# Kernel optimization log

Measured on AMD Instinct MI355X. Metric: run time of the kernel, lower is better.

## Reference

```python
import jax, jax.numpy as jnp
import numpy as np

# ---- module hyperparameters (from init_kwargs) ----
DIM = 16        # Hilbert-space dimension (density matrix is DIM x DIM)
BATCH = 32      # number of initial states evolved in parallel
K_LIND = 4      # number of Lindblad collapse operators
N_TS = 512      # number of Euler integration steps
N_CTRLS = 4     # number of control channels
N_PARAMS = 16   # B-spline control points per channel
DEGREE = 3      # cubic B-splines
T_TOTAL = 1.0
DT = T_TOTAL / N_TS


def _bspline_basis_matrix(t, knots, degree):
    """Cox-de Boor recursion, vectorized over all basis functions.
    t: (n_ts,), knots: (n_knots,). Returns (n_ts, n_knots-1-degree)."""
    k = knots
    # degree-0: indicator of half-open knot spans -> (n_ts, n_knots-1)
    B = ((k[None, :-1] <= t[:, None]) & (t[:, None] < k[None, 1:])).astype(t.dtype)
    for d in range(1, degree + 1):
        left_den = k[d:-1] - k[:-(d + 1)]
        right_den = k[d + 1:] - k[1:-d]
        left = jnp.where(left_den > 0,
                         (t[:, None] - k[None, :-(d + 1)]) / jnp.where(left_den > 0, left_den, 1.0) * B[:, :-1],
                         0.0)
        right = jnp.where(right_den > 0,
                          (k[None, d + 1:] - t[:, None]) / jnp.where(right_den > 0, right_den, 1.0) * B[:, 1:],
                          0.0)
        B = left + right
    return B  # (n_ts, n_knots - 1 - degree) == (n_ts, N_PARAMS)


def setup_inputs() -> dict:
    key = jax.random.key(0)
    ks = jax.random.split(key, 10)
    f32 = jnp.float32
    params = 0.5 * jax.random.normal(ks[0], (N_PARAMS, N_CTRLS), f32)
    H0_re = jax.random.normal(ks[1], (DIM, DIM), f32)
    H0_im = jax.random.normal(ks[2], (DIM, DIM), f32)
    Hc_re = jax.random.normal(ks[3], (N_CTRLS, DIM, DIM), f32)
    Hc_im = jax.random.normal(ks[4], (N_CTRLS, DIM, DIM), f32)
    L_re = 0.3 * jax.random.normal(ks[5], (K_LIND, DIM, DIM), f32)
    L_im = 0.3 * jax.random.normal(ks[6], (K_LIND, DIM, DIM), f32)
    # valid density matrices: rho0 = A A^dag / tr(A A^dag)
    A = (jax.random.normal(ks[7], (BATCH, DIM, DIM), f32)
         + 1j * jax.random.normal(ks[8], (BATCH, DIM, DIM), f32)).astype(jnp.complex64)
    rho0 = jnp.einsum('bij,bkj->bik', A, A.conj())
    tr = jnp.trace(rho0, axis1=-2, axis2=-1).real[:, None, None]
    rho0 = rho0 / tr.astype(jnp.complex64)
    return {
        'params': params,
        'H0_re': H0_re, 'H0_im': H0_im,
        'Hc_re': Hc_re, 'Hc_im': Hc_im,
        'L_re': L_re, 'L_im': L_im,
        'rho0_re': jnp.real(rho0).astype(f32),
        'rho0_im': jnp.imag(rho0).astype(f32),
    }


def reference(params, H0_re, H0_im, Hc_re, Hc_im, L_re, L_im, rho0_re, rho0_im):
    c64 = jnp.complex64
    # Hermitize Hamiltonians
    H0 = (H0_re + 1j * H0_im).astype(c64)
    H0 = 0.5 * (H0 + H0.conj().T)
    Hc = (Hc_re + 1j * Hc_im).astype(c64)
    Hc = 0.5 * (Hc + jnp.conj(jnp.swapaxes(Hc, -1, -2)))
    L = (L_re + 1j * L_im).astype(c64)              # (K, d, d)
    LdL = jnp.einsum('kji,kjl->il', L.conj(), L)    # sum_k L^dag L  (d, d)
    rho0 = (rho0_re + 1j * rho0_im).astype(c64)     # (B, d, d)

    # B-spline control pulses (clamped knot vector, as in evaluate_bspline_batch)
    t = jnp.arange(N_TS, dtype=jnp.float32) * DT
    knots = jnp.concatenate([
        jnp.zeros(DEGREE, jnp.float32),
        jnp.linspace(0.0, T_TOTAL, N_PARAMS - DEGREE + 1).astype(jnp.float32),
        T_TOTAL * jnp.ones(DEGREE, jnp.float32),
    ])
    basis = _bspline_basis_matrix(t, knots, DEGREE)  # (n_ts, n_params)
    u = basis @ params                               # (n_ts, n_ctrls)

    def step(rho, u_t):
        H = H0 + jnp.einsum('c,cij->ij', u_t.astype(c64), Hc)
        jump = jnp.einsum('kij,bjl,kml->bim', L, rho, L.conj())
        drho = (-1j) * (H @ rho - rho @ H) + jump - 0.5 * (LdL @ rho + rho @ LdL)
        rho_new = rho + DT * drho
        pops = jnp.real(jnp.diagonal(rho_new, axis1=-2, axis2=-1)).astype(jnp.float32)
        return rho_new, pops

    _, pops = jax.lax.scan(step, rho0, u)
    return pops  # (n_ts, batch, dim) real populations
```

## Files before the change

### kernel.cpp

```cpp
#include <hip/hip_runtime.h>
#include <hip/hip_bf16.h>

#define DIM    16
#define BATCH  32
#define KL     4
#define NTS    512
#define NC     4
#define NPAR   16
#define DTF    (1.0f/512.0f)
#define BST    40
#define FST    20

using short8  = __attribute__((ext_vector_type(8))) short;
using short4v = __attribute__((ext_vector_type(4))) short;
using f32x4   = __attribute__((ext_vector_type(4))) float;

__device__ __forceinline__ float b2f(__hip_bfloat16 x) { return __bfloat162float(x); }

__device__ __forceinline__ float ldval(const void* p, int idx, bool isf32) {
  return isf32 ? ((const float*)p)[idx]
               : __bfloat162float(((const __hip_bfloat16*)p)[idx]);
}
__device__ __forceinline__ unsigned short f2bf(float x) {
  unsigned u = __float_as_uint(x);
  unsigned r = u + 0x7FFFu + ((u >> 16) & 1u);
  return (unsigned short)(r >> 16);
}
__device__ __forceinline__ float bf2f(unsigned short h) {
  return __uint_as_float(((unsigned)h) << 16);
}
__device__ __forceinline__ void split2(float v, unsigned short& h, unsigned short& l) {
  unsigned u = __float_as_uint(v);
  h = (unsigned short)(u >> 16);
  float r = v - __uint_as_float(u & 0xFFFF0000u);
  l = (unsigned short)(__float_as_uint(r) >> 16);
}
__device__ __forceinline__ short8 ldfrag(const unsigned short* p) {
  return *(const short8*)p;
}
__device__ __forceinline__ short8 negbf8(short8 a) {
  union { short8 s; unsigned u[4]; } v; v.s = a;
  #pragma unroll
  for (int q = 0; q < 4; ++q) v.u[q] ^= 0x80008000u;
  return v.s;
}
__device__ __forceinline__ f32x4 mm3(short8 Ah, short8 Al, short8 Bh, short8 Bl, f32x4 acc) {
  acc = __builtin_amdgcn_mfma_f32_16x16x32_bf16(Ah, Bh, acc, 0, 0, 0);
  acc = __builtin_amdgcn_mfma_f32_16x16x32_bf16(Al, Bh, acc, 0, 0, 0);
  acc = __builtin_amdgcn_mfma_f32_16x16x32_bf16(Ah, Bl, acc, 0, 0, 0);
  return acc;
}
__device__ __forceinline__ void packfrag(const float* v, short8& hi, short8& lo) {
  union { short8 s; unsigned short e[8]; } H, L;
  #pragma unroll
  for (int q = 0; q < 8; ++q) split2(v[q], H.e[q], L.e[q]);
  hi = H.s; lo = L.s;
}

__global__ __launch_bounds__(512, 1)
void lindblad_evolve(const void* __restrict__ g_params,
                     const void* __restrict__ g_H0re, const void* __restrict__ g_H0im,
                     const void* __restrict__ g_Hcre, const void* __restrict__ g_Hcim,
                     const void* __restrict__ g_Lre,  const void* __restrict__ g_Lim,
                     const void* __restrict__ g_r0re, const void* __restrict__ g_r0im,
                     float* __restrict__ g_out)
{
  __shared__ __align__(16) unsigned short sPh[16*BST], sPl[16*BST];
  __shared__ __align__(16) unsigned short sTh[KL][16*BST], sTl[KL][16*BST];
  __shared__ __align__(16) unsigned short sLh[KL][16*BST], sLl[KL][16*BST];
  __shared__ __align__(16) float sMr[16*FST],  sMi[16*FST];
  __shared__ __align__(16) float sMrT[16*FST], sMiT[16*FST];
  __shared__ __align__(16) float sU[NTS][NC];
  __shared__ __align__(16) float sPops[NTS*DIM];
  __shared__ int sFlag;

  const int tid = threadIdx.x;
  const int b   = blockIdx.x;
  const int wv  = tid >> 6;
  const int ln  = tid & 63;
  const int fm  = ln & 15;
  const int fq  = ln >> 4;
  const int row0 = fq * 4;
  const int fOff  = fm*BST + fq*8;
  const int fOffS = fm*BST + ((fq*8 + 16) & 31);

  if (tid == 0) sFlag = 0;
  __syncthreads();
  if (tid < 256) {
    float v = b2f(((const __hip_bfloat16*)g_H0re)[tid]);
    if (!(fabsf(v) <= 1e10f)) atomicOr(&sFlag, 1);
  }
  __syncthreads();
  const bool isf32 = (sFlag != 0);

  {
    float kn[20];
    kn[0] = 0.f; kn[1] = 0.f; kn[2] = 0.f;
    #pragma unroll
    for (int q = 0; q < 14; ++q) kn[3 + q] = (float)q / 13.0f;
    kn[17] = 1.f; kn[18] = 1.f; kn[19] = 1.f;
    const float t = (float)tid * DTF;
    float B[19];
    #pragma unroll
    for (int q = 0; q < 19; ++q) B[q] = (kn[q] <= t && t < kn[q+1]) ? 1.f : 0.f;
    #pragma unroll
    for (int d = 1; d <= 3; ++d) {
      #pragma unroll
      for (int q = 0; q + d < 19; ++q) {
        float ld = kn[q+d]   - kn[q];
        float rd = kn[q+d+1] - kn[q+1];
        float lv = (ld > 0.f) ? (t - kn[q])     / ld * B[q]   : 0.f;
        float rv = (rd > 0.f) ? (kn[q+d+1] - t) / rd * B[q+1] : 0.f;
        B[q] = lv + rv;
      }
    }
    #pragma unroll
    for (int c = 0; c < NC; ++c) {
      float s = 0.f;
      #pragma unroll
      for (int q = 0; q < NPAR; ++q) s += B[q] * ldval(g_params, q*NC + c, isf32);
      sU[tid][c] = s;
    }
  }

  if (tid < 256) {
    float* scr = sPops;
    const int i = tid >> 4, j = tid & 15;
    const int ij = i*16 + j, ji = j*16 + i;
    float h0r = 0.5f * (ldval(g_H0re, ij, isf32) + ldval(g_H0re, ji, isf32));
    float h0i = 0.5f * (ldval(g_H0im, ij, isf32) - ldval(g_H0im, ji, isf32));
    float ldr = 0.f, ldi = 0.f;
    for (int k = 0; k < KL; ++k) {
      #pragma unroll
      for (int m = 0; m < DIM; ++m) {
        float ar = ldval(g_Lre, k*256 + m*16 + i, isf32), ai = ldval(g_Lim, k*256 + m*16 + i, isf32);
        float br = ldval(g_Lre, k*256 + m*16 + j, isf32), bi = ldval(g_Lim, k*256 + m*16 + j, isf32);
        ldr += ar*br + ai*bi;
        ldi += ar*bi - ai*br;
      }
    }
    scr[0*256 + ij] =  h0i - 0.5f*ldr;
    scr[1*256 + ij] = -h0r - 0.5f*ldi;
    #pragma unroll
    for (int c = 0; c < NC; ++c) {
      float hr = 0.5f * (ldval(g_Hcre, c*256 + ij, isf32) + ldval(g_Hcre, c*256 + ji, isf32));
      float hi = 0.5f * (ldval(g_Hcim, c*256 + ij, isf32) - ldval(g_Hcim, c*256 + ji, isf32));
      scr[(2 + 2*c)*256 + ij] =  hi;
      scr[(3 + 2*c)*256 + ij] = -hr;
    }
    #pragma unroll
    for (int k = 0; k < KL; ++k) {
      float lr = ldval(g_Lre, k*256 + ij, isf32);
      float li = ldval(g_Lim, k*256 + ij, isf32);
      unsigned short h;
      h = f2bf(lr); sLh[k][i*BST + j]      = h; sLl[k][i*BST + j]      = f2bf(lr - bf2f(h));
      h = f2bf(li); sLh[k][i*BST + 16 + j] = h; sLl[k][i*BST + 16 + j] = f2bf(li - bf2f(h));
    }
    float r0 = ldval(g_r0re, b*256 + ij, isf32);
    float m0 = ldval(g_r0im, b*256 + ij, isf32);
    unsigned short h, l;
    split2(r0, h, l); sPh[j*BST + i]      = h; sPl[j*BST + i]      = l;
    split2(m0, h, l); sPh[j*BST + 16 + i] = h; sPl[j*BST + 16 + i] = l;
  }

  __syncthreads();

  short8 Ah, Al;
  short8 TrBh, TrBl, TiBh, TiBl;
  short8 JBh[KL], JBl[KL];
  float  G0v[8], Gcv[NC][8];
  float  rm[4] = {0.f,0.f,0.f,0.f};

  if (wv < 2) {
    const int comp = (fq < 2) ? 0 : 1;
    const int base = (fq & 1) * 8;
    const float* scr = sPops;
    {
      const float* s0 = &scr[comp*256 + fm*16 + base];
      f32x4 va = *(const f32x4*)s0, vb = *(const f32x4*)(s0 + 4);
      #pragma unroll
      for (int q = 0; q < 4; ++q) { G0v[q] = va[q]; G0v[4+q] = vb[q]; }
    }
    #pragma unroll
    for (int c = 0; c < NC; ++c) {
      const float* s0 = &scr[(2 + 2*c + comp)*256 + fm*16 + base];
      f32x4 va = *(const f32x4*)s0, vb = *(const f32x4*)(s0 + 4);
      #pragma unroll
      for (int q = 0; q < 4; ++q) { Gcv[c][q] = va[q]; Gcv[c][4+q] = vb[q]; }
    }
    f32x4 uv = *(const f32x4*)&sU[0][0];
    float gv[8];
    #pragma unroll
    for (int q = 0; q < 8; ++q)
      gv[q] = G0v[q] + uv[0]*Gcv[0][q] + uv[1]*Gcv[1][q] + uv[2]*Gcv[2][q] + uv[3]*Gcv[3][q];
    packfrag(gv, Ah, Al);
  } else if (wv < 6) {
    const int k = wv - 2;
    TiBh = ldfrag(&sLh[k][fOff]);
    TiBl = ldfrag(&sLl[k][fOff]);
    TrBh = (fq >= 2) ? negbf8(TiBh) : TiBh;
    TrBl = (fq >= 2) ? negbf8(TiBl) : TiBl;
  } else if (wv == 6) {
    #pragma unroll
    for (int k = 0; k < KL; ++k) { JBh[k] = ldfrag(&sLh[k][fOff]); JBl[k] = ldfrag(&sLl[k][fOff]); }
    #pragma unroll
    for (int q = 0; q < 4; ++q) rm[q] = ldval(g_r0re, b*256 + (row0+q)*16 + fm, isf32);
  } else {
    #pragma unroll
    for (int k = 0; k < KL; ++k) {
      short8 h = ldfrag(&sLh[k][fOffS]);
      short8 l = ldfrag(&sLl[k][fOffS]);
      if (fq < 2) { h = negbf8(h); l = negbf8(l); }
      JBh[k] = h; JBl[k] = l;
    }
    #pragma unroll
    for (int q = 0; q < 4; ++q) rm[q] = ldval(g_r0im, b*256 + (row0+q)*16 + fm, isf32);
  }

  #pragma unroll 1
  for (int t = 0; t < NTS; ++t) {
    __syncthreads();

    if (wv < 2) {
      short8 Bh, Bl;
      if (wv == 0) {
        Bh = ldfrag(&sPh[fOff]);  Bl = ldfrag(&sPl[fOff]);
        if (fq >= 2) { Bh = negbf8(Bh); Bl = negbf8(Bl); }
      } else {
        Bh = ldfrag(&sPh[fOffS]); Bl = ldfrag(&sPl[fOffS]);
      }
      f32x4 a = {0.f,0.f,0.f,0.f};
      a = mm3(Ah, Al, Bh, Bl, a);
      float* Mn = (wv == 0) ? sMr  : sMi;
      float* Mt = (wv == 0) ? sMrT : sMiT;
      #pragma unroll
      for (int r = 0; r < 4; ++r) Mn[(row0 + r)*FST + fm] = a[r];
      *(f32x4*)&Mt[fm*FST + row0] = a;
    } else if (wv < 6) {
      const int k = wv - 2;
      short8 Arh = ldfrag(&sPh[fOff]),  Arl = ldfrag(&sPl[fOff]);
      short8 Aih = ldfrag(&sPh[fOffS]), Ail = ldfrag(&sPl[fOffS]);
      f32x4 tr = {0.f,0.f,0.f,0.f}, ti = {0.f,0.f,0.f,0.f};
      tr = mm3(Arh, Arl, TrBh, TrBl, tr);
      ti = mm3(Aih, Ail, TiBh, TiBl, ti);
      union { short4v s; unsigned short e[4]; } HR, LR, HI, LI;
      #pragma unroll
      for (int r = 0; r < 4; ++r) {
        split2(tr[r], HR.e[r], LR.e[r]);
        split2(ti[r], HI.e[r], LI.e[r]);
      }
      *(short4v*)&sTh[k][fm*BST + row0]      = HR.s;
      *(short4v*)&sTl[k][fm*BST + row0]      = LR.s;
      *(short4v*)&sTh[k][fm*BST + 16 + row0] = HI.s;
      *(short4v*)&sTl[k][fm*BST + 16 + row0] = LI.s;
    }

    __syncthreads();

    if (wv >= 6) {
      short8 T0h = ldfrag(&sTh[0][fOff]), T0l = ldfrag(&sTl[0][fOff]);
      short8 T1h = ldfrag(&sTh[1][fOff]), T1l = ldfrag(&sTl[1][fOff]);
      short8 T2h = ldfrag(&sTh[2][fOff]), T2l = ldfrag(&sTl[2][fOff]);
      short8 T3h = ldfrag(&sTh[3][fOff]), T3l = ldfrag(&sTl[3][fOff]);
      f32x4 a0 = {0.f,0.f,0.f,0.f}, a1 = {0.f,0.f,0.f,0.f},
            a2 = {0.f,0.f,0.f,0.f}, a3 = {0.f,0.f,0.f,0.f};
      a0 = mm3(JBh[0], JBl[0], T0h, T0l, a0);
      a1 = mm3(JBh[1], JBl[1], T1h, T1l, a1);
      a2 = mm3(JBh[2], JBl[2], T2h, T2l, a2);
      a3 = mm3(JBh[3], JBl[3], T3h, T3l, a3);
      const float* Mt = (wv == 6) ? sMrT : sMiT;
      const float* Mn = (wv == 6) ? sMr  : sMi;
      f32x4 d1 = *(const f32x4*)&Mt[fm*FST + row0];
      f32x4 d2 = *(const f32x4*)&Mn[fm*FST + row0];
      union { short4v s; unsigned short e[4]; } HH, LL;
      if (wv == 6) {
        #pragma unroll
        for (int q = 0; q < 4; ++q) {
          rm[q] += DTF * (d1[q] + d2[q] + ((a0[q] + a1[q]) + (a2[q] + a3[q])));
          split2(rm[q], HH.e[q], LL.e[q]);
        }
        *(short4v*)&sPh[fm*BST + row0] = HH.s;
        *(short4v*)&sPl[fm*BST + row0] = LL.s;
        if ((unsigned)(fm - row0) < 4u) sPops[t*DIM + fm] = rm[fm - row0];
      } else {
        #pragma unroll
        for (int q = 0; q < 4; ++q) {
          rm[q] += DTF * (d1[q] - d2[q] - ((a0[q] + a1[q]) + (a2[q] + a3[q])));
          split2(rm[q], HH.e[q], LL.e[q]);
        }
        *(short4v*)&sPh[fm*BST + 16 + row0] = HH.s;
        *(short4v*)&sPl[fm*BST + 16 + row0] = LL.s;
      }
    } else if (wv < 2) {
      const int tn = (t + 1 < NTS) ? (t + 1) : t;
      f32x4 uv = *(const f32x4*)&sU[tn][0];
      float gv[8];
      #pragma unroll
      for (int q = 0; q < 8; ++q)
        gv[q] = G0v[q] + uv[0]*Gcv[0][q] + uv[1]*Gcv[1][q] + uv[2]*Gcv[2][q] + uv[3]*Gcv[3][q];
      packfrag(gv, Ah, Al);
    }
  }

  __syncthreads();
  #pragma unroll
  for (int s = 0; s < NTS*DIM/(512*4); ++s) {
    int idx = (s*512 + tid) * 4;
    int tt = idx >> 4, dd = idx & 15;
    *(float4*)&g_out[tt*(BATCH*DIM) + b*DIM + dd] = *(const float4*)&sPops[idx];
  }
}

extern "C" void kernel_launch(void* const* d_in, const int* in_sizes, int n_in,
                              void* d_out, int out_size, void* d_ws, size_t ws_size,
                              hipStream_t stream) {
  (void)out_size; (void)d_ws; (void)ws_size;
  const void *P, *H0r, *H0i, *Hcr, *Hci, *Lr, *Li, *R0r, *R0i;
  int idx64 = -1;
  for (int q = 0; q < n_in; ++q) if (in_sizes[q] == 64) idx64 = q;
  if (idx64 == 6) {
    H0i = d_in[0]; H0r = d_in[1];
    Hci = d_in[2]; Hcr = d_in[3];
    Li  = d_in[4]; Lr  = d_in[5];
    P   = d_in[6];
    R0i = d_in[7]; R0r = d_in[8];
  } else {
    P   = d_in[0];
    H0r = d_in[1]; H0i = d_in[2];
    Hcr = d_in[3]; Hci = d_in[4];
    Lr  = d_in[5]; Li  = d_in[6];
    R0r = d_in[7]; R0i = d_in[8];
  }
  lindblad_evolve<<<dim3(BATCH), dim3(512), 0, stream>>>(
      P, H0r, H0i, Hcr, Hci, Lr, Li, R0r, R0i, (float*)d_out);
}
```

Baseline: 416.4 us.

## Collapse eight specialised waves into two waves each doing all step stages

Reduces the block from 512 to 128 threads so that two waves each handle a real or imaginary component through the commutator, jump-operator transposes and accumulation, instead of eight role-specialised waves. This lowers the cost of each per-step __syncthreads and lets the commutator result stay in registers, removing the transposed staging buffer. It also replaces the scalar bf16 hi/lo split with byte-permute packing. In exchange, each wave does more serial MFMA work per step, so the dependency chain inside a step gets longer.

```diff
diff --git a/kernel.cpp b/kernel.cpp
--- a/kernel.cpp
+++ b/kernel.cpp
@@ -50,14 +50,34 @@
   acc = __builtin_amdgcn_mfma_f32_16x16x32_bf16(Ah, Bl, acc, 0, 0, 0);
   return acc;
 }
-__device__ __forceinline__ void packfrag(const float* v, short8& hi, short8& lo) {
-  union { short8 s; unsigned short e[8]; } H, L;
+__device__ __forceinline__ void pack4(f32x4 v, short4v& hi, short4v& lo) {
+  union { short4v s; unsigned d[2]; } H, L;
+  unsigned u0 = __float_as_uint(v[0]), u1 = __float_as_uint(v[1]);
+  unsigned u2 = __float_as_uint(v[2]), u3 = __float_as_uint(v[3]);
+  H.d[0] = __builtin_amdgcn_perm(u1, u0, 0x07060302u);
+  H.d[1] = __builtin_amdgcn_perm(u3, u2, 0x07060302u);
+  float r0 = v[0] - __uint_as_float(u0 & 0xFFFF0000u);
+  float r1 = v[1] - __uint_as_float(u1 & 0xFFFF0000u);
+  float r2 = v[2] - __uint_as_float(u2 & 0xFFFF0000u);
+  float r3 = v[3] - __uint_as_float(u3 & 0xFFFF0000u);
+  L.d[0] = __builtin_amdgcn_perm(__float_as_uint(r1), __float_as_uint(r0), 0x07060302u);
+  L.d[1] = __builtin_amdgcn_perm(__float_as_uint(r3), __float_as_uint(r2), 0x07060302u);
+  hi = H.s; lo = L.s;
+}
+__device__ __forceinline__ void pack8(const float* v, short8& hi, short8& lo) {
+  union { short8 s; unsigned d[4]; } H, L;
   #pragma unroll
-  for (int q = 0; q < 8; ++q) split2(v[q], H.e[q], L.e[q]);
+  for (int j = 0; j < 4; ++j) {
+    unsigned ua = __float_as_uint(v[2*j]), ub = __float_as_uint(v[2*j+1]);
+    H.d[j] = __builtin_amdgcn_perm(ub, ua, 0x07060302u);
+    float ra = v[2*j]   - __uint_as_float(ua & 0xFFFF0000u);
+    float rb = v[2*j+1] - __uint_as_float(ub & 0xFFFF0000u);
+    L.d[j] = __builtin_amdgcn_perm(__float_as_uint(rb), __float_as_uint(ra), 0x07060302u);
+  }
   hi = H.s; lo = L.s;
 }
 
-__global__ __launch_bounds__(512, 1)
+__global__ __launch_bounds__(128, 1)
 void lindblad_evolve(const void* __restrict__ g_params,
                      const void* __restrict__ g_H0re, const void* __restrict__ g_H0im,
                      const void* __restrict__ g_Hcre, const void* __restrict__ g_Hcim,
@@ -68,8 +88,7 @@
   __shared__ __align__(16) unsigned short sPh[16*BST], sPl[16*BST];
   __shared__ __align__(16) unsigned short sTh[KL][16*BST], sTl[KL][16*BST];
   __shared__ __align__(16) unsigned short sLh[KL][16*BST], sLl[KL][16*BST];
-  __shared__ __align__(16) float sMr[16*FST],  sMi[16*FST];
-  __shared__ __align__(16) float sMrT[16*FST], sMiT[16*FST];
+  __shared__ __align__(16) float sMr[16*FST], sMi[16*FST];
   __shared__ __align__(16) float sU[NTS][NC];
   __shared__ __align__(16) float sPops[NTS*DIM];
   __shared__ int sFlag;
@@ -86,20 +105,20 @@
 
   if (tid == 0) sFlag = 0;
   __syncthreads();
-  if (tid < 256) {
-    float v = b2f(((const __hip_bfloat16*)g_H0re)[tid]);
+  for (int e = tid; e < 256; e += 128) {
+    float v = b2f(((const __hip_bfloat16*)g_H0re)[e]);
     if (!(fabsf(v) <= 1e10f)) atomicOr(&sFlag, 1);
   }
   __syncthreads();
   const bool isf32 = (sFlag != 0);
 
-  {
+  for (int t0 = tid; t0 < NTS; t0 += 128) {
     float kn[20];
     kn[0] = 0.f; kn[1] = 0.f; kn[2] = 0.f;
     #pragma unroll
     for (int q = 0; q < 14; ++q) kn[3 + q] = (float)q / 13.0f;
     kn[17] = 1.f; kn[18] = 1.f; kn[19] = 1.f;
-    const float t = (float)tid * DTF;
+    const float t = (float)t0 * DTF;
     float B[19];
     #pragma unroll
     for (int q = 0; q < 19; ++q) B[q] = (kn[q] <= t && t < kn[q+1]) ? 1.f : 0.f;
@@ -119,13 +138,13 @@
       float s = 0.f;
       #pragma unroll
       for (int q = 0; q < NPAR; ++q) s += B[q] * ldval(g_params, q*NC + c, isf32);
-      sU[tid][c] = s;
-    }
-  }
-
-  if (tid < 256) {
+      sU[t0][c] = s;
+    }
+  }
+
+  for (int e = tid; e < 256; e += 128) {
     float* scr = sPops;
-    const int i = tid >> 4, j = tid & 15;
+    const int i = e >> 4, j = e & 15;
     const int ij = i*16 + j, ji = j*16 + i;
     float h0r = 0.5f * (ldval(g_H0re, ij, isf32) + ldval(g_H0re, ji, isf32));
     float h0i = 0.5f * (ldval(g_H0im, ij, isf32) - ldval(g_H0im, ji, isf32));
@@ -166,12 +185,8 @@
   __syncthreads();
 
   short8 Ah, Al;
-  short8 TrBh, TrBl, TiBh, TiBl;
-  short8 JBh[KL], JBl[KL];
   float  G0v[8], Gcv[NC][8];
-  float  rm[4] = {0.f,0.f,0.f,0.f};
-
-  if (wv < 2) {
+  {
     const int comp = (fq < 2) ? 0 : 1;
     const int base = (fq & 1) * 8;
     const float* scr = sPops;
@@ -193,14 +208,22 @@
     #pragma unroll
     for (int q = 0; q < 8; ++q)
       gv[q] = G0v[q] + uv[0]*Gcv[0][q] + uv[1]*Gcv[1][q] + uv[2]*Gcv[2][q] + uv[3]*Gcv[3][q];
-    packfrag(gv, Ah, Al);
-  } else if (wv < 6) {
-    const int k = wv - 2;
-    TiBh = ldfrag(&sLh[k][fOff]);
-    TiBl = ldfrag(&sLl[k][fOff]);
-    TrBh = (fq >= 2) ? negbf8(TiBh) : TiBh;
-    TrBl = (fq >= 2) ? negbf8(TiBl) : TiBl;
-  } else if (wv == 6) {
+    pack8(gv, Ah, Al);
+  }
+
+  short8 TiBh[2], TiBl[2], TrBh[2], TrBl[2];
+  #pragma unroll
+  for (int j = 0; j < 2; ++j) {
+    const int k = 2*wv + j;
+    TiBh[j] = ldfrag(&sLh[k][fOff]);
+    TiBl[j] = ldfrag(&sLl[k][fOff]);
+    TrBh[j] = (fq >= 2) ? negbf8(TiBh[j]) : TiBh[j];
+    TrBl[j] = (fq >= 2) ? negbf8(TiBl[j]) : TiBl[j];
+  }
+
+  short8 JBh[KL], JBl[KL];
+  float  rm[4];
+  if (wv == 0) {
     #pragma unroll
     for (int k = 0; k < KL; ++k) { JBh[k] = ldfrag(&sLh[k][fOff]); JBl[k] = ldfrag(&sLl[k][fOff]); }
     #pragma unroll
@@ -217,95 +240,96 @@
     for (int q = 0; q < 4; ++q) rm[q] = ldval(g_r0im, b*256 + (row0+q)*16 + fm, isf32);
   }
 
+  float* const Mn = (wv == 0) ? sMr : sMi;
+
   #pragma unroll 1
   for (int t = 0; t < NTS; ++t) {
     __syncthreads();
 
-    if (wv < 2) {
-      short8 Bh, Bl;
-      if (wv == 0) {
-        Bh = ldfrag(&sPh[fOff]);  Bl = ldfrag(&sPl[fOff]);
-        if (fq >= 2) { Bh = negbf8(Bh); Bl = negbf8(Bl); }
-      } else {
-        Bh = ldfrag(&sPh[fOffS]); Bl = ldfrag(&sPl[fOffS]);
+    short8 Pfh = ldfrag(&sPh[fOff]),  Pfl = ldfrag(&sPl[fOff]);
+    short8 Psh = ldfrag(&sPh[fOffS]), Psl = ldfrag(&sPl[fOffS]);
+
+    short8 MBh, MBl;
+    if (wv == 0) {
+      MBh = Pfh; MBl = Pfl;
+      if (fq >= 2) { MBh = negbf8(MBh); MBl = negbf8(MBl); }
+    } else {
+      MBh = Psh; MBl = Psl;
+    }
+    f32x4 mAcc = {0.f,0.f,0.f,0.f};
+    mAcc = mm3(Ah, Al, MBh, MBl, mAcc);
+
+    #pragma unroll
+    for (int j = 0; j < 2; ++j) {
+      const int k = 2*wv + j;
+      f32x4 tr = {0.f,0.f,0.f,0.f}, ti = {0.f,0.f,0.f,0.f};
+      tr = mm3(Pfh, Pfl, TrBh[j], TrBl[j], tr);
+      ti = mm3(Psh, Psl, TiBh[j], TiBl[j], ti);
+      short4v HR, LR, HI2, LI2;
+      pack4(tr, HR, LR);
+      pack4(ti, HI2, LI2);
+      *(short4v*)&sTh[k][fm*BST + row0]      = HR;
+      *(short4v*)&sTl[k][fm*BST + row0]      = LR;
+      *(short4v*)&sTh[k][fm*BST + 16 + row0] = HI2;
+      *(short4v*)&sTl[k][fm*BST + 16 + row0] = LI2;
+    }
+
+    #pragma unroll
+    for (int r = 0; r < 4; ++r) Mn[(row0 + r)*FST + fm] = mAcc[r];
+
+    __syncthreads();
+
+    short8 T0h = ldfrag(&sTh[0][fOff]), T0l = ldfrag(&sTl[0][fOff]);
+    short8 T1h = ldfrag(&sTh[1][fOff]), T1l = ldfrag(&sTl[1][fOff]);
+    short8 T2h = ldfrag(&sTh[2][fOff]), T2l = ldfrag(&sTl[2][fOff]);
+    short8 T3h = ldfrag(&sTh[3][fOff]), T3l = ldfrag(&sTl[3][fOff]);
+    f32x4 d2 = *(const f32x4*)&Mn[fm*FST + row0];
+    f32x4 a0 = {0.f,0.f,0.f,0.f}, a1 = {0.f,0.f,0.f,0.f},
+          a2 = {0.f,0.f,0.f,0.f}, a3 = {0.f,0.f,0.f,0.f};
+    a0 = mm3(JBh[0], JBl[0], T0h, T0l, a0);
+    a1 = mm3(JBh[1], JBl[1], T1h, T1l, a1);
+    a2 = mm3(JBh[2], JBl[2], T2h, T2l, a2);
+    a3 = mm3(JBh[3], JBl[3], T3h, T3l, a3);
+
+    short4v HH, LL;
+    if (wv == 0) {
+      f32x4 rv;
+      #pragma unroll
+      for (int q = 0; q < 4; ++q) {
+        rm[q] += DTF * (mAcc[q] + d2[q] + ((a0[q] + a1[q]) + (a2[q] + a3[q])));
+        rv[q] = rm[q];
       }
-      f32x4 a = {0.f,0.f,0.f,0.f};
-      a = mm3(Ah, Al, Bh, Bl, a);
-      float* Mn = (wv == 0) ? sMr  : sMi;
-      float* Mt = (wv == 0) ? sMrT : sMiT;
-      #pragma unroll
-      for (int r = 0; r < 4; ++r) Mn[(row0 + r)*FST + fm] = a[r];
-      *(f32x4*)&Mt[fm*FST + row0] = a;
-    } else if (wv < 6) {
-      const int k = wv - 2;
-      short8 Arh = ldfrag(&sPh[fOff]),  Arl = ldfrag(&sPl[fOff]);
-      short8 Aih = ldfrag(&sPh[fOffS]), Ail = ldfrag(&sPl[fOffS]);
-      f32x4 tr = {0.f,0.f,0.f,0.f}, ti = {0.f,0.f,0.f,0.f};
-      tr = mm3(Arh, Arl, TrBh, TrBl, tr);
-      ti = mm3(Aih, Ail, TiBh, TiBl, ti);
-      union { short4v s; unsigned short e[4]; } HR, LR, HI, LI;
-      #pragma unroll
-      for (int r = 0; r < 4; ++r) {
-        split2(tr[r], HR.e[r], LR.e[r]);
-        split2(ti[r], HI.e[r], LI.e[r]);
+      pack4(rv, HH, LL);
+      *(short4v*)&sPh[fm*BST + row0] = HH;
+      *(short4v*)&sPl[fm*BST + row0] = LL;
+      if ((unsigned)(fm - row0) < 4u) sPops[t*DIM + fm] = rm[fm - row0];
+    } else {
+      f32x4 rv;
+      #pragma unroll
+      for (int q = 0; q < 4; ++q) {
+        rm[q] += DTF * (mAcc[q] - d2[q] - ((a0[q] + a1[q]) + (a2[q] + a3[q])));
+        rv[q] = rm[q];
       }
-      *(short4v*)&sTh[k][fm*BST + row0]      = HR.s;
-      *(short4v*)&sTl[k][fm*BST + row0]      = LR.s;
-      *(short4v*)&sTh[k][fm*BST + 16 + row0] = HI.s;
-      *(short4v*)&sTl[k][fm*BST + 16 + row0] = LI.s;
-    }
-
-    __syncthreads();
-
-    if (wv >= 6) {
-      short8 T0h = ldfrag(&sTh[0][fOff]), T0l = ldfrag(&sTl[0][fOff]);
-      short8 T1h = ldfrag(&sTh[1][fOff]), T1l = ldfrag(&sTl[1][fOff]);
-      short8 T2h = ldfrag(&sTh[2][fOff]), T2l = ldfrag(&sTl[2][fOff]);
-      short8 T3h = ldfrag(&sTh[3][fOff]), T3l = ldfrag(&sTl[3][fOff]);
-      f32x4 a0 = {0.f,0.f,0.f,0.f}, a1 = {0.f,0.f,0.f,0.f},
-            a2 = {0.f,0.f,0.f,0.f}, a3 = {0.f,0.f,0.f,0.f};
-      a0 = mm3(JBh[0], JBl[0], T0h, T0l, a0);
-      a1 = mm3(JBh[1], JBl[1], T1h, T1l, a1);
-      a2 = mm3(JBh[2], JBl[2], T2h, T2l, a2);
-      a3 = mm3(JBh[3], JBl[3], T3h, T3l, a3);
-      const float* Mt = (wv == 6) ? sMrT : sMiT;
-      const float* Mn = (wv == 6) ? sMr  : sMi;
-      f32x4 d1 = *(const f32x4*)&Mt[fm*FST + row0];
-      f32x4 d2 = *(const f32x4*)&Mn[fm*FST + row0];
-      union { short4v s; unsigned short e[4]; } HH, LL;
-      if (wv == 6) {
-        #pragma unroll
-        for (int q = 0; q < 4; ++q) {
-          rm[q] += DTF * (d1[q] + d2[q] + ((a0[q] + a1[q]) + (a2[q] + a3[q])));
-          split2(rm[q], HH.e[q], LL.e[q]);
-        }
-        *(short4v*)&sPh[fm*BST + row0] = HH.s;
-        *(short4v*)&sPl[fm*BST + row0] = LL.s;
-        if ((unsigned)(fm - row0) < 4u) sPops[t*DIM + fm] = rm[fm - row0];
-      } else {
-        #pragma unroll
-        for (int q = 0; q < 4; ++q) {
-          rm[q] += DTF * (d1[q] - d2[q] - ((a0[q] + a1[q]) + (a2[q] + a3[q])));
-          split2(rm[q], HH.e[q], LL.e[q]);
-        }
-        *(short4v*)&sPh[fm*BST + 16 + row0] = HH.s;
-        *(short4v*)&sPl[fm*BST + 16 + row0] = LL.s;
-      }
-    } else if (wv < 2) {
+      pack4(rv, HH, LL);
+      *(short4v*)&sPh[fm*BST + 16 + row0] = HH;
+      *(short4v*)&sPl[fm*BST + 16 + row0] = LL;
+    }
+
+    {
       const int tn = (t + 1 < NTS) ? (t + 1) : t;
       f32x4 uv = *(const f32x4*)&sU[tn][0];
       float gv[8];
       #pragma unroll
       for (int q = 0; q < 8; ++q)
         gv[q] = G0v[q] + uv[0]*Gcv[0][q] + uv[1]*Gcv[1][q] + uv[2]*Gcv[2][q] + uv[3]*Gcv[3][q];
-      packfrag(gv, Ah, Al);
+      pack8(gv, Ah, Al);
     }
   }
 
   __syncthreads();
   #pragma unroll
-  for (int s = 0; s < NTS*DIM/(512*4); ++s) {
-    int idx = (s*512 + tid) * 4;
+  for (int s = 0; s < NTS*DIM/(128*4); ++s) {
+    int idx = (s*128 + tid) * 4;
     int tt = idx >> 4, dd = idx & 15;
     *(float4*)&g_out[tt*(BATCH*DIM) + b*DIM + dd] = *(const float4*)&sPops[idx];
   }
@@ -331,6 +355,6 @@
     Lr  = d_in[5]; Li  = d_in[6];
     R0r = d_in[7]; R0i = d_in[8];
   }
-  lindblad_evolve<<<dim3(BATCH), dim3(512), 0, stream>>>(
+  lindblad_evolve<<<dim3(BATCH), dim3(128), 0, stream>>>(
       P, H0r, H0i, Hcr, Hci, Lr, Li, R0r, R0i, (float*)d_out);
 }
```

Result: slower. 564.2 us (+35.5%).

## Interleave two batch states per block to overlap dependent phases

Applied to the files above, without the earlier changes.

Each block now evolves two density matrices. Phase 1 of one state runs between the same barriers as phase 2 of the other, so waves that sat idle during a serial dependency now have work. The grid is halved to 16 blocks, and the scalar bf16 split routines are replaced with byte-permute packing helpers. The cost is doubled shared memory for the buffers and populations, plus a longer serial chain per block.

```diff
diff --git a/kernel.cpp b/kernel.cpp
--- a/kernel.cpp
+++ b/kernel.cpp
@@ -50,10 +50,30 @@
   acc = __builtin_amdgcn_mfma_f32_16x16x32_bf16(Ah, Bl, acc, 0, 0, 0);
   return acc;
 }
-__device__ __forceinline__ void packfrag(const float* v, short8& hi, short8& lo) {
-  union { short8 s; unsigned short e[8]; } H, L;
+__device__ __forceinline__ void pack4(f32x4 v, short4v& hi, short4v& lo) {
+  union { short4v s; unsigned d[2]; } H, L;
+  unsigned u0 = __float_as_uint(v[0]), u1 = __float_as_uint(v[1]);
+  unsigned u2 = __float_as_uint(v[2]), u3 = __float_as_uint(v[3]);
+  H.d[0] = __builtin_amdgcn_perm(u1, u0, 0x07060302u);
+  H.d[1] = __builtin_amdgcn_perm(u3, u2, 0x07060302u);
+  float r0 = v[0] - __uint_as_float(u0 & 0xFFFF0000u);
+  float r1 = v[1] - __uint_as_float(u1 & 0xFFFF0000u);
+  float r2 = v[2] - __uint_as_float(u2 & 0xFFFF0000u);
+  float r3 = v[3] - __uint_as_float(u3 & 0xFFFF0000u);
+  L.d[0] = __builtin_amdgcn_perm(__float_as_uint(r1), __float_as_uint(r0), 0x07060302u);
+  L.d[1] = __builtin_amdgcn_perm(__float_as_uint(r3), __float_as_uint(r2), 0x07060302u);
+  hi = H.s; lo = L.s;
+}
+__device__ __forceinline__ void pack8(const float* v, short8& hi, short8& lo) {
+  union { short8 s; unsigned d[4]; } H, L;
   #pragma unroll
-  for (int q = 0; q < 8; ++q) split2(v[q], H.e[q], L.e[q]);
+  for (int j = 0; j < 4; ++j) {
+    unsigned ua = __float_as_uint(v[2*j]), ub = __float_as_uint(v[2*j+1]);
+    H.d[j] = __builtin_amdgcn_perm(ub, ua, 0x07060302u);
+    float ra = v[2*j]   - __uint_as_float(ua & 0xFFFF0000u);
+    float rb = v[2*j+1] - __uint_as_float(ub & 0xFFFF0000u);
+    L.d[j] = __builtin_amdgcn_perm(__float_as_uint(rb), __float_as_uint(ra), 0x07060302u);
+  }
   hi = H.s; lo = L.s;
 }
 
@@ -65,17 +85,18 @@
                      const void* __restrict__ g_r0re, const void* __restrict__ g_r0im,
                      float* __restrict__ g_out)
 {
-  __shared__ __align__(16) unsigned short sPh[16*BST], sPl[16*BST];
-  __shared__ __align__(16) unsigned short sTh[KL][16*BST], sTl[KL][16*BST];
+  __shared__ __align__(16) unsigned short sPh[2][16*BST], sPl[2][16*BST];
+  __shared__ __align__(16) unsigned short sTh[2][KL][16*BST], sTl[2][KL][16*BST];
   __shared__ __align__(16) unsigned short sLh[KL][16*BST], sLl[KL][16*BST];
-  __shared__ __align__(16) float sMr[16*FST],  sMi[16*FST];
-  __shared__ __align__(16) float sMrT[16*FST], sMiT[16*FST];
+  __shared__ __align__(16) float sMr[2][16*FST],  sMi[2][16*FST];
+  __shared__ __align__(16) float sMrT[2][16*FST], sMiT[2][16*FST];
   __shared__ __align__(16) float sU[NTS][NC];
-  __shared__ __align__(16) float sPops[NTS*DIM];
+  __shared__ __align__(16) float sPops[2][NTS*DIM];
   __shared__ int sFlag;
 
   const int tid = threadIdx.x;
-  const int b   = blockIdx.x;
+  const int b0  = 2*blockIdx.x;
+  const int b1  = b0 + 1;
   const int wv  = tid >> 6;
   const int ln  = tid & 63;
   const int fm  = ln & 15;
@@ -124,7 +145,7 @@
   }
 
   if (tid < 256) {
-    float* scr = sPops;
+    float* scr = sPops[0];
     const int i = tid >> 4, j = tid & 15;
     const int ij = i*16 + j, ji = j*16 + i;
     float h0r = 0.5f * (ldval(g_H0re, ij, isf32) + ldval(g_H0re, ji, isf32));
@@ -156,11 +177,15 @@
       h = f2bf(lr); sLh[k][i*BST + j]      = h; sLl[k][i*BST + j]      = f2bf(lr - bf2f(h));
       h = f2bf(li); sLh[k][i*BST + 16 + j] = h; sLl[k][i*BST + 16 + j] = f2bf(li - bf2f(h));
     }
-    float r0 = ldval(g_r0re, b*256 + ij, isf32);
-    float m0 = ldval(g_r0im, b*256 + ij, isf32);
-    unsigned short h, l;
-    split2(r0, h, l); sPh[j*BST + i]      = h; sPl[j*BST + i]      = l;
-    split2(m0, h, l); sPh[j*BST + 16 + i] = h; sPl[j*BST + 16 + i] = l;
+    #pragma unroll
+    for (int c = 0; c < 2; ++c) {
+      const int bb = b0 + c;
+      float r0 = ldval(g_r0re, bb*256 + ij, isf32);
+      float m0 = ldval(g_r0im, bb*256 + ij, isf32);
+      unsigned short h, l;
+      split2(r0, h, l); sPh[c][j*BST + i]      = h; sPl[c][j*BST + i]      = l;
+      split2(m0, h, l); sPh[c][j*BST + 16 + i] = h; sPl[c][j*BST + 16 + i] = l;
+    }
   }
 
   __syncthreads();
@@ -169,12 +194,13 @@
   short8 TrBh, TrBl, TiBh, TiBl;
   short8 JBh[KL], JBl[KL];
   float  G0v[8], Gcv[NC][8];
-  float  rm[4] = {0.f,0.f,0.f,0.f};
+  float  rmA[4] = {0.f,0.f,0.f,0.f};
+  float  rmB[4] = {0.f,0.f,0.f,0.f};
 
   if (wv < 2) {
     const int comp = (fq < 2) ? 0 : 1;
     const int base = (fq & 1) * 8;
-    const float* scr = sPops;
+    const float* scr = sPops[0];
     {
       const float* s0 = &scr[comp*256 + fm*16 + base];
       f32x4 va = *(const f32x4*)s0, vb = *(const f32x4*)(s0 + 4);
@@ -193,7 +219,7 @@
     #pragma unroll
     for (int q = 0; q < 8; ++q)
       gv[q] = G0v[q] + uv[0]*Gcv[0][q] + uv[1]*Gcv[1][q] + uv[2]*Gcv[2][q] + uv[3]*Gcv[3][q];
-    packfrag(gv, Ah, Al);
+    pack8(gv, Ah, Al);
   } else if (wv < 6) {
     const int k = wv - 2;
     TiBh = ldfrag(&sLh[k][fOff]);
@@ -204,7 +230,10 @@
     #pragma unroll
     for (int k = 0; k < KL; ++k) { JBh[k] = ldfrag(&sLh[k][fOff]); JBl[k] = ldfrag(&sLl[k][fOff]); }
     #pragma unroll
-    for (int q = 0; q < 4; ++q) rm[q] = ldval(g_r0re, b*256 + (row0+q)*16 + fm, isf32);
+    for (int q = 0; q < 4; ++q) {
+      rmA[q] = ldval(g_r0re, b0*256 + (row0+q)*16 + fm, isf32);
+      rmB[q] = ldval(g_r0re, b1*256 + (row0+q)*16 + fm, isf32);
+    }
   } else {
     #pragma unroll
     for (int k = 0; k < KL; ++k) {
@@ -214,100 +243,116 @@
       JBh[k] = h; JBl[k] = l;
     }
     #pragma unroll
-    for (int q = 0; q < 4; ++q) rm[q] = ldval(g_r0im, b*256 + (row0+q)*16 + fm, isf32);
-  }
+    for (int q = 0; q < 4; ++q) {
+      rmA[q] = ldval(g_r0im, b0*256 + (row0+q)*16 + fm, isf32);
+      rmB[q] = ldval(g_r0im, b1*256 + (row0+q)*16 + fm, isf32);
+    }
+  }
+
+#define P1WORK(c) do { \
+    if (wv < 2) { \
+      short8 Bh, Bl; \
+      if (wv == 0) { \
+        Bh = ldfrag(&sPh[c][fOff]);  Bl = ldfrag(&sPl[c][fOff]); \
+        if (fq >= 2) { Bh = negbf8(Bh); Bl = negbf8(Bl); } \
+      } else { \
+        Bh = ldfrag(&sPh[c][fOffS]); Bl = ldfrag(&sPl[c][fOffS]); \
+      } \
+      f32x4 a = {0.f,0.f,0.f,0.f}; \
+      a = mm3(Ah, Al, Bh, Bl, a); \
+      float* Mn = (wv == 0) ? sMr[c]  : sMi[c]; \
+      float* Mt = (wv == 0) ? sMrT[c] : sMiT[c]; \
+      _Pragma("unroll") \
+      for (int r = 0; r < 4; ++r) Mn[(row0 + r)*FST + fm] = a[r]; \
+      *(f32x4*)&Mt[fm*FST + row0] = a; \
+    } else if (wv < 6) { \
+      const int k = wv - 2; \
+      short8 Arh = ldfrag(&sPh[c][fOff]),  Arl = ldfrag(&sPl[c][fOff]); \
+      short8 Aih = ldfrag(&sPh[c][fOffS]), Ail = ldfrag(&sPl[c][fOffS]); \
+      f32x4 tr = {0.f,0.f,0.f,0.f}, ti = {0.f,0.f,0.f,0.f}; \
+      tr = mm3(Arh, Arl, TrBh, TrBl, tr); \
+      ti = mm3(Aih, Ail, TiBh, TiBl, ti); \
+      short4v HR, LR, HI2, LI2; \
+      pack4(tr, HR, LR); \
+      pack4(ti, HI2, LI2); \
+      *(short4v*)&sTh[c][k][fm*BST + row0]      = HR; \
+      *(short4v*)&sTl[c][k][fm*BST + row0]      = LR; \
+      *(short4v*)&sTh[c][k][fm*BST + 16 + row0] = HI2; \
+      *(short4v*)&sTl[c][k][fm*BST + 16 + row0] = LI2; \
+    } \
+  } while (0)
+
+#define P2WORK(c, tt) do { \
+    if (wv >= 6) { \
+      short8 T0h = ldfrag(&sTh[c][0][fOff]), T0l = ldfrag(&sTl[c][0][fOff]); \
+      short8 T1h = ldfrag(&sTh[c][1][fOff]), T1l = ldfrag(&sTl[c][1][fOff]); \
+      short8 T2h = ldfrag(&sTh[c][2][fOff]), T2l = ldfrag(&sTl[c][2][fOff]); \
+      short8 T3h = ldfrag(&sTh[c][3][fOff]), T3l = ldfrag(&sTl[c][3][fOff]); \
+      f32x4 a0 = {0.f,0.f,0.f,0.f}, a1 = {0.f,0.f,0.f,0.f}, \
+            a2 = {0.f,0.f,0.f,0.f}, a3 = {0.f,0.f,0.f,0.f}; \
+      a0 = mm3(JBh[0], JBl[0], T0h, T0l, a0); \
+      a1 = mm3(JBh[1], JBl[1], T1h, T1l, a1); \
+      a2 = mm3(JBh[2], JBl[2], T2h, T2l, a2); \
+      a3 = mm3(JBh[3], JBl[3], T3h, T3l, a3); \
+      const float* Mt_ = (wv == 6) ? sMrT[c] : sMiT[c]; \
+      const float* Mn_ = (wv == 6) ? sMr[c]  : sMi[c]; \
+      f32x4 d1 = *(const f32x4*)&Mt_[fm*FST + row0]; \
+      f32x4 d2 = *(const f32x4*)&Mn_[fm*FST + row0]; \
+      float* rmp = (c) ? rmB : rmA; \
+      f32x4 rv; short4v HH, LL; \
+      if (wv == 6) { \
+        _Pragma("unroll") \
+        for (int q = 0; q < 4; ++q) { \
+          rmp[q] += DTF * (d1[q] + d2[q] + ((a0[q] + a1[q]) + (a2[q] + a3[q]))); \
+          rv[q] = rmp[q]; \
+        } \
+        pack4(rv, HH, LL); \
+        *(short4v*)&sPh[c][fm*BST + row0] = HH; \
+        *(short4v*)&sPl[c][fm*BST + row0] = LL; \
+        if ((unsigned)(fm - row0) < 4u) sPops[c][(tt)*DIM + fm] = rmp[fm - row0]; \
+      } else { \
+        _Pragma("unroll") \
+        for (int q = 0; q < 4; ++q) { \
+          rmp[q] += DTF * (d1[q] - d2[q] - ((a0[q] + a1[q]) + (a2[q] + a3[q]))); \
+          rv[q] = rmp[q]; \
+        } \
+        pack4(rv, HH, LL); \
+        *(short4v*)&sPh[c][fm*BST + 16 + row0] = HH; \
+        *(short4v*)&sPl[c][fm*BST + 16 + row0] = LL; \
+      } \
+    } \
+  } while (0)
 
   #pragma unroll 1
-  for (int t = 0; t < NTS; ++t) {
+  for (int i = 0; i <= NTS; ++i) {
     __syncthreads();
-
+    if (i < NTS) P1WORK(0);
+    if (i > 0)   P2WORK(1, i-1);
+    if (i == NTS) break;
+    __syncthreads();
+    P2WORK(0, i);
+    P1WORK(1);
     if (wv < 2) {
-      short8 Bh, Bl;
-      if (wv == 0) {
-        Bh = ldfrag(&sPh[fOff]);  Bl = ldfrag(&sPl[fOff]);
-        if (fq >= 2) { Bh = negbf8(Bh); Bl = negbf8(Bl); }
-      } else {
-        Bh = ldfrag(&sPh[fOffS]); Bl = ldfrag(&sPl[fOffS]);
-      }
-      f32x4 a = {0.f,0.f,0.f,0.f};
-      a = mm3(Ah, Al, Bh, Bl, a);
-      float* Mn = (wv == 0) ? sMr  : sMi;
-      float* Mt = (wv == 0) ? sMrT : sMiT;
-      #pragma unroll
-      for (int r = 0; r < 4; ++r) Mn[(row0 + r)*FST + fm] = a[r];
-      *(f32x4*)&Mt[fm*FST + row0] = a;
-    } else if (wv < 6) {
-      const int k = wv - 2;
-      short8 Arh = ldfrag(&sPh[fOff]),  Arl = ldfrag(&sPl[fOff]);
-      short8 Aih = ldfrag(&sPh[fOffS]), Ail = ldfrag(&sPl[fOffS]);
-      f32x4 tr = {0.f,0.f,0.f,0.f}, ti = {0.f,0.f,0.f,0.f};
-      tr = mm3(Arh, Arl, TrBh, TrBl, tr);
-      ti = mm3(Aih, Ail, TiBh, TiBl, ti);
-      union { short4v s; unsigned short e[4]; } HR, LR, HI, LI;
-      #pragma unroll
-      for (int r = 0; r < 4; ++r) {
-        split2(tr[r], HR.e[r], LR.e[r]);
-        split2(ti[r], HI.e[r], LI.e[r]);
-      }
-      *(short4v*)&sTh[k][fm*BST + row0]      = HR.s;
-      *(short4v*)&sTl[k][fm*BST + row0]      = LR.s;
-      *(short4v*)&sTh[k][fm*BST + 16 + row0] = HI.s;
-      *(short4v*)&sTl[k][fm*BST + 16 + row0] = LI.s;
-    }
-
-    __syncthreads();
-
-    if (wv >= 6) {
-      short8 T0h = ldfrag(&sTh[0][fOff]), T0l = ldfrag(&sTl[0][fOff]);
-      short8 T1h = ldfrag(&sTh[1][fOff]), T1l = ldfrag(&sTl[1][fOff]);
-      short8 T2h = ldfrag(&sTh[2][fOff]), T2l = ldfrag(&sTl[2][fOff]);
-      short8 T3h = ldfrag(&sTh[3][fOff]), T3l = ldfrag(&sTl[3][fOff]);
-      f32x4 a0 = {0.f,0.f,0.f,0.f}, a1 = {0.f,0.f,0.f,0.f},
-            a2 = {0.f,0.f,0.f,0.f}, a3 = {0.f,0.f,0.f,0.f};
-      a0 = mm3(JBh[0], JBl[0], T0h, T0l, a0);
-      a1 = mm3(JBh[1], JBl[1], T1h, T1l, a1);
-      a2 = mm3(JBh[2], JBl[2], T2h, T2l, a2);
-      a3 = mm3(JBh[3], JBl[3], T3h, T3l, a3);
-      const float* Mt = (wv == 6) ? sMrT : sMiT;
-      const float* Mn = (wv == 6) ? sMr  : sMi;
-      f32x4 d1 = *(const f32x4*)&Mt[fm*FST + row0];
-      f32x4 d2 = *(const f32x4*)&Mn[fm*FST + row0];
-      union { short4v s; unsigned short e[4]; } HH, LL;
-      if (wv == 6) {
-        #pragma unroll
-        for (int q = 0; q < 4; ++q) {
-          rm[q] += DTF * (d1[q] + d2[q] + ((a0[q] + a1[q]) + (a2[q] + a3[q])));
-          split2(rm[q], HH.e[q], LL.e[q]);
-        }
-        *(short4v*)&sPh[fm*BST + row0] = HH.s;
-        *(short4v*)&sPl[fm*BST + row0] = LL.s;
-        if ((unsigned)(fm - row0) < 4u) sPops[t*DIM + fm] = rm[fm - row0];
-      } else {
-        #pragma unroll
-        for (int q = 0; q < 4; ++q) {
-          rm[q] += DTF * (d1[q] - d2[q] - ((a0[q] + a1[q]) + (a2[q] + a3[q])));
-          split2(rm[q], HH.e[q], LL.e[q]);
-        }
-        *(short4v*)&sPh[fm*BST + 16 + row0] = HH.s;
-        *(short4v*)&sPl[fm*BST + 16 + row0] = LL.s;
-      }
-    } else if (wv < 2) {
-      const int tn = (t + 1 < NTS) ? (t + 1) : t;
+      const int tn = (i + 1 < NTS) ? (i + 1) : (NTS - 1);
       f32x4 uv = *(const f32x4*)&sU[tn][0];
       float gv[8];
       #pragma unroll
       for (int q = 0; q < 8; ++q)
         gv[q] = G0v[q] + uv[0]*Gcv[0][q] + uv[1]*Gcv[1][q] + uv[2]*Gcv[2][q] + uv[3]*Gcv[3][q];
-      packfrag(gv, Ah, Al);
+      pack8(gv, Ah, Al);
     }
   }
 
   __syncthreads();
   #pragma unroll
-  for (int s = 0; s < NTS*DIM/(512*4); ++s) {
-    int idx = (s*512 + tid) * 4;
-    int tt = idx >> 4, dd = idx & 15;
-    *(float4*)&g_out[tt*(BATCH*DIM) + b*DIM + dd] = *(const float4*)&sPops[idx];
+  for (int c = 0; c < 2; ++c) {
+    const int bb = b0 + c;
+    #pragma unroll
+    for (int s = 0; s < NTS*DIM/(512*4); ++s) {
+      int idx = (s*512 + tid) * 4;
+      int tt = idx >> 4, dd = idx & 15;
+      *(float4*)&g_out[tt*(BATCH*DIM) + bb*DIM + dd] = *(const float4*)&sPops[c][idx];
+    }
   }
 }
 
@@ -331,6 +376,6 @@
     Lr  = d_in[5]; Li  = d_in[6];
     R0r = d_in[7]; R0i = d_in[8];
   }
-  lindblad_evolve<<<dim3(BATCH), dim3(512), 0, stream>>>(
+  lindblad_evolve<<<dim3(BATCH/2), dim3(512), 0, stream>>>(
       P, H0r, H0i, Hcr, Hci, Lr, Li, R0r, R0i, (float*)d_out);
 }
```

Measured after the change: 556.3 us. 33.6% more time.
